# Performance work log

Measured on AMD Instinct MI355X. Metric: run time of the kernel, lower is better.

Reference implementation:

```python
import jax, jax.numpy as jnp
import numpy as np

KERNEL = 9
STRIDE = 2
NUM_ITERS = 3


def squash(s):
    # Matches the module: norm over last dim; v = ||s|| / (1 + ||s||^2) * s
    n = jnp.linalg.norm(s, axis=-1, keepdims=True)
    return n / (1.0 + n * n) * s


def setup_inputs() -> dict:
    key = jax.random.key(0)
    k1, k2, k3 = jax.random.split(key, 3)
    B, nc, ic, oc, H = 32, 32, 256, 32, 71  # H'=(71-9)//2+1 = 32 = B = nc = oc (required by the original broadcasting)
    x = jax.random.normal(k1, (B, ic, H, H), dtype=jnp.float32)
    # Conv2d default init: U(-1/sqrt(fan_in), 1/sqrt(fan_in)), fan_in = ic*9*9
    bound = 1.0 / np.sqrt(ic * KERNEL * KERNEL)
    W = jax.random.uniform(k2, (nc, oc, ic, KERNEL, KERNEL), jnp.float32, -bound, bound)
    b = jax.random.uniform(k3, (nc, oc), jnp.float32, -bound, bound)
    return {"x": x, "W": W, "b": b}


def reference(x, W, b):
    nc, oc, ic = W.shape[0], W.shape[1], W.shape[2]
    # All nc per-capsule convs fused into one grouped output-channel conv
    Wf = W.reshape(nc * oc, ic, KERNEL, KERNEL)
    u = jax.lax.conv_general_dilated(
        x, Wf, window_strides=(STRIDE, STRIDE), padding='VALID',
        dimension_numbers=('NCHW', 'OIHW', 'NCHW'))
    B = u.shape[0]
    Hp, Wp = u.shape[2], u.shape[3]
    u_hat = u.reshape(B, nc, oc, Hp, Wp) + b[None, :, :, None, None]  # [B,nc,oc,Hp,Wp]

    # Dynamic routing. The torch code initializes b_ij as rank-4 zeros; because
    # softmax(0) is uniform and 0 + agreement == agreement, this rank-5 zero init
    # is numerically identical and shape-clean.
    b_ij = jnp.zeros((B, nc, oc, Hp, 1), dtype=u_hat.dtype)
    v = None
    for it in range(NUM_ITERS):
        c = jax.nn.softmax(b_ij, axis=1)                  # over capsule dim
        s = (c * u_hat).sum(axis=2, keepdims=True)        # [B,nc,1,Hp,Wp]
        v = squash(s)
        if it < NUM_ITERS - 1:
            b_ij = b_ij + (u_hat * v).sum(axis=-1, keepdims=True)  # [B,nc,oc,Hp,1]
    # torch returns v_j.squeeze(-1): last dim is Wp != 1 so it is a no-op
    return v  # [B, nc, 1, Hp, Wp]
```

## Files before the change

### kernel.cpp

```cpp
#include <hip/hip_runtime.h>
#include <cstdint>
#include <cstddef>

typedef unsigned short u16;
typedef signed char s8;
typedef __attribute__((ext_vector_type(4))) int i32x4;

#define XT_HSTRIDE 18432
#define XT_BSTRIDE 1308672
#define K_TOT 20736
#define N_TOT 32768
#define NKT 324
#define S_X (5.0f / 127.0f)

__device__ __forceinline__ u16 f2bf(float f) {
  uint32_t u = __builtin_bit_cast(uint32_t, f);
  u = (u + 0x7fffu + ((u >> 16) & 1u)) >> 16;
  return (u16)u;
}
__device__ __forceinline__ float bf2f(u16 h) {
  uint32_t u = ((uint32_t)h) << 16;
  return __builtin_bit_cast(float, u);
}

__device__ __forceinline__ void gl_lds16(const s8* g, s8* l) {
  __builtin_amdgcn_global_load_lds((const __attribute__((address_space(1))) void*)g,
                                   (__attribute__((address_space(3))) void*)l, 16, 0, 0);
}

__device__ __forceinline__ void wg_barrier() {
  asm volatile("" ::: "memory");
  __builtin_amdgcn_s_barrier();
  asm volatile("" ::: "memory");
}

__device__ __forceinline__ void koffs(int kt, int& ka, int& kb) {
  const int pos = kt >> 2;
  const int cq = kt & 3;
  const int kh = pos / 9;
  const int kw = pos - kh * 9;
  ka = kt * 64;
  kb = kh * XT_HSTRIDE + (kw & 1) * 9216 + (kw >> 1) * 256 + cq * 64;
}

__global__ __launch_bounds__(256) void pack_w(const float* __restrict__ W,
                                              s8* __restrict__ Wb,
                                              float* __restrict__ sw) {
  __shared__ __align__(16) s8 wl[81 * 264];
  __shared__ float red[256];
  const int m = blockIdx.x;
  const int t = threadIdx.x;
  const size_t base = (size_t)m * K_TOT;
  float r[81];
  float mx = 0.f;
#pragma unroll
  for (int k = 0; k < 81; ++k) {
    r[k] = W[base + t + k * 256];
    mx = fmaxf(mx, fabsf(r[k]));
  }
  red[t] = mx;
  __syncthreads();
  for (int s = 128; s > 0; s >>= 1) {
    if (t < s) red[t] = fmaxf(red[t], red[t + s]);
    __syncthreads();
  }
  const float amax = fmaxf(red[0], 1e-20f);
  const float inv = 127.0f / amax;
  if (t == 0) sw[m] = amax * (1.0f / 127.0f);
#pragma unroll
  for (int k = 0; k < 81; ++k) {
    const int i = t + k * 256;
    const int c = i / 81;
    const int pos = i - c * 81;
    wl[pos * 264 + c] = (s8)__float2int_rn(r[k] * inv);
  }
  __syncthreads();
  for (int idx = t; idx < 81 * 32; idx += 256) {
    const int pos = idx >> 5;
    const int cq = idx & 31;
    *(uint2*)(Wb + base + pos * 256 + cq * 8) =
        *(const uint2*)(wl + pos * 264 + cq * 8);
  }
}

__global__ __launch_bounds__(256) void pack_x(const float* __restrict__ X,
                                              s8* __restrict__ xT) {
  __shared__ s8 xl[71 * 260];
  const int h = blockIdx.x;
  const int b = blockIdx.y;
  const int t = threadIdx.x;
  for (int i = t; i < 256 * 71; i += 256) {
    int c = i / 71;
    int w = i - c * 71;
    float f = X[(((size_t)(b * 256 + c)) * 71 + h) * 71 + w];
    f = fminf(fmaxf(f, -5.f), 5.f) * 25.4f;
    xl[w * 260 + c] = (s8)__float2int_rn(f);
  }
  __syncthreads();
  const size_t obase = (size_t)b * XT_BSTRIDE + (size_t)h * XT_HSTRIDE;
  const int c4 = t & 63;
  const int g = t >> 6;
  for (int s = g; s < 71; s += 4) {
    int par = (s >= 36) ? 1 : 0;
    int j = s - par * 36;
    int w = 2 * j + par;
    uint32_t d = *(const uint32_t*)&xl[w * 260 + 4 * c4];
    *(uint32_t*)&xT[obase + par * 9216 + j * 256 + 4 * c4] = d;
  }
}

__global__ __launch_bounds__(512, 2) void conv_gemm(const s8* __restrict__ Wb,
                                                    const s8* __restrict__ xT,
                                                    const float* __restrict__ sw,
                                                    u16* __restrict__ U) {
  __shared__ __align__(16) s8 As[2][2][256 * 64];
  __shared__ __align__(16) s8 Bs[2][2][256 * 64];
  const int tid = threadIdx.x;
  const int bx = blockIdx.x;
  const int swz = (bx & 7) * 64 + (bx >> 3);
  const int m0 = (swz & 3) * 256;
  const int n0 = (swz >> 2) * 256;
  const int lane = tid & 63;
  const int wave = tid >> 6;
  const int wm = wave >> 2;
  const int wn = wave & 3;

  const int rl2 = lane >> 2;
  const int gch16 = ((lane & 3) ^ ((rl2 >> 1) & 3)) * 16;

  const s8* aS[2];
  const s8* bS[2];
#pragma unroll
  for (int j = 0; j < 2; ++j) {
    const int row = j * 128 + wave * 16 + rl2;
    aS[j] = Wb + (size_t)(m0 + row) * K_TOT + gch16;
    const int n = n0 + row;
    const size_t nb = (size_t)(n >> 10) * XT_BSTRIDE +
                      (size_t)(((n >> 5) & 31) * 2) * XT_HSTRIDE +
                      (size_t)(n & 31) * 256;
    bS[j] = xT + nb + gch16;
  }
  const int sdst = wave * 16 * 64 + lane * 16;

  i32x4 acc[8][4];
#pragma unroll
  for (int i = 0; i < 8; ++i)
#pragma unroll
    for (int j = 0; j < 4; ++j) acc[i][j] = (i32x4){0, 0, 0, 0};

  const int fr = lane & 15;
  const int q4 = lane >> 4;
  const int cph = ((q4 ^ ((fr >> 1) & 3))) * 16;
  int offA[8], offB[4];
#pragma unroll
  for (int mi = 0; mi < 8; ++mi)
    offA[mi] = (wm * 128 + (mi & 3) * 16 + (mi >> 2) * 64 + fr) * 64 + cph;
#pragma unroll
  for (int j = 0; j < 4; ++j)
    offB[j] = (wn * 64 + j * 16 + fr) * 64 + cph;

  {
    int ka0, kb0, ka1, kb1;
    koffs(0, ka0, kb0);
    koffs(1, ka1, kb1);
    gl_lds16(bS[0] + kb0, &Bs[0][0][0 * 8192 + sdst]);
    gl_lds16(bS[1] + kb0, &Bs[0][0][1 * 8192 + sdst]);
    gl_lds16(bS[0] + kb1, &Bs[0][1][0 * 8192 + sdst]);
    gl_lds16(bS[1] + kb1, &Bs[0][1][1 * 8192 + sdst]);
    gl_lds16(aS[0] + ka0, &As[0][0][0 * 8192 + sdst]);
    gl_lds16(aS[1] + ka0, &As[0][0][1 * 8192 + sdst]);
    gl_lds16(aS[0] + ka1, &As[0][1][0 * 8192 + sdst]);
    gl_lds16(aS[1] + ka1, &As[0][1][1 * 8192 + sdst]);
  }

#pragma unroll 1
  for (int it2 = 0; it2 < NKT / 2; ++it2) {
    const int sp = it2 & 1;
    const bool more = (it2 + 1 < NKT / 2);
    int ka0n = 0, kb0n = 0, ka1n = 0, kb1n = 0;
    if (more) {
      koffs(2 * it2 + 2, ka0n, kb0n);
      koffs(2 * it2 + 3, ka1n, kb1n);
    }
    const s8* Ac0 = &As[sp][0][0];
    const s8* Bc0 = &Bs[sp][0][0];
    const s8* Ac1 = &As[sp][1][0];
    const s8* Bc1 = &Bs[sp][1][0];
    s8* An0 = &As[sp ^ 1][0][0];
    s8* Bn0 = &Bs[sp ^ 1][0][0];
    s8* An1 = &As[sp ^ 1][1][0];
    s8* Bn1 = &Bs[sp ^ 1][1][0];

    asm volatile("s_waitcnt vmcnt(0)" ::: "memory");
    wg_barrier();

    i32x4 aF[8], bF[4];

#pragma unroll
    for (int j = 0; j < 4; ++j) bF[j] = *(const i32x4*)(Bc0 + offB[j]);
#pragma unroll
    for (int mi = 0; mi < 4; ++mi) aF[mi] = *(const i32x4*)(Ac0 + offA[mi]);
    if (more) {
      gl_lds16(bS[0] + kb0n, Bn0 + 0 * 8192 + sdst);
      gl_lds16(bS[1] + kb0n, Bn0 + 1 * 8192 + sdst);
    }
    __builtin_amdgcn_s_setprio(1);
#pragma unroll
    for (int mi = 0; mi < 4; ++mi)
#pragma unroll
      for (int j = 0; j < 4; ++j)
        acc[mi][j] = __builtin_amdgcn_mfma_i32_16x16x64_i8(aF[mi], bF[j], acc[mi][j], 0, 0, 0);
    __builtin_amdgcn_s_setprio(0);
    __builtin_amdgcn_sched_barrier(0);

#pragma unroll
    for (int mi = 4; mi < 8; ++mi) aF[mi] = *(const i32x4*)(Ac0 + offA[mi]);
    if (more) {
      gl_lds16(bS[0] + kb1n, Bn1 + 0 * 8192 + sdst);
      gl_lds16(bS[1] + kb1n, Bn1 + 1 * 8192 + sdst);
    }
    __builtin_amdgcn_s_setprio(1);
#pragma unroll
    for (int mi = 4; mi < 8; ++mi)
#pragma unroll
      for (int j = 0; j < 4; ++j)
        acc[mi][j] = __builtin_amdgcn_mfma_i32_16x16x64_i8(aF[mi], bF[j], acc[mi][j], 0, 0, 0);
    __builtin_amdgcn_s_setprio(0);
    __builtin_amdgcn_sched_barrier(0);

#pragma unroll
    for (int j = 0; j < 4; ++j) bF[j] = *(const i32x4*)(Bc1 + offB[j]);
#pragma unroll
    for (int mi = 0; mi < 4; ++mi) aF[mi] = *(const i32x4*)(Ac1 + offA[mi]);
    if (more) {
      gl_lds16(aS[0] + ka0n, An0 + 0 * 8192 + sdst);
      gl_lds16(aS[1] + ka0n, An0 + 1 * 8192 + sdst);
    }
    __builtin_amdgcn_s_setprio(1);
#pragma unroll
    for (int mi = 0; mi < 4; ++mi)
#pragma unroll
      for (int j = 0; j < 4; ++j)
        acc[mi][j] = __builtin_amdgcn_mfma_i32_16x16x64_i8(aF[mi], bF[j], acc[mi][j], 0, 0, 0);
    __builtin_amdgcn_s_setprio(0);
    __builtin_amdgcn_sched_barrier(0);

#pragma unroll
    for (int mi = 4; mi < 8; ++mi) aF[mi] = *(const i32x4*)(Ac1 + offA[mi]);
    if (more) {
      gl_lds16(aS[0] + ka1n, An1 + 0 * 8192 + sdst);
      gl_lds16(aS[1] + ka1n, An1 + 1 * 8192 + sdst);
    }
    __builtin_amdgcn_s_setprio(1);
#pragma unroll
    for (int mi = 4; mi < 8; ++mi)
#pragma unroll
      for (int j = 0; j < 4; ++j)
        acc[mi][j] = __builtin_amdgcn_mfma_i32_16x16x64_i8(aF[mi], bF[j], acc[mi][j], 0, 0, 0);
    __builtin_amdgcn_s_setprio(0);
  }

  const int r0 = (lane >> 4) * 4;
  const int cn = lane & 15;
#pragma unroll
  for (int mi = 0; mi < 8; ++mi) {
    const int mgb = m0 + wm * 128 + (mi & 3) * 16 + (mi >> 2) * 64 + r0;
    float ds[4];
#pragma unroll
    for (int r = 0; r < 4; ++r) ds[r] = sw[mgb + r] * S_X;
#pragma unroll
    for (int j = 0; j < 4; ++j) {
      const int ng = n0 + wn * 64 + j * 16 + cn;
#pragma unroll
      for (int r = 0; r < 4; ++r)
        U[(size_t)(mgb + r) * N_TOT + ng] = f2bf((float)acc[mi][j][r] * ds[r]);
    }
  }
}

__global__ __launch_bounds__(1024) void routing_k(const u16* __restrict__ U,
                                                  const float* __restrict__ bias,
                                                  float* __restrict__ out) {
  const int t = threadIdx.x;
  const int bx = blockIdx.x;
  const int b = bx >> 5;
  const int hp = bx & 31;
  const int oc = t & 31;
  __shared__ float sm[1024];

  float u_r[32];
  {
    const uint4* up4 = (const uint4*)(U + (size_t)t * N_TOT + b * 1024 + hp * 32);
    const float bs = bias[t];
#pragma unroll
    for (int i = 0; i < 4; ++i) {
      uint4 q = up4[i];
      uint32_t vv[4] = {q.x, q.y, q.z, q.w};
#pragma unroll
      for (int k = 0; k < 4; ++k) {
        u_r[i * 8 + k * 2]     = bf2f((u16)(vv[k] & 0xffffu)) + bs;
        u_r[i * 8 + k * 2 + 1] = bf2f((u16)(vv[k] >> 16)) + bs;
      }
    }
  }

  float bij = 0.f;
  float s[32];
  float scale = 0.f;

  {
    const float c = 1.0f / 32.0f;
#pragma unroll
    for (int w = 0; w < 32; ++w) s[w] = c * u_r[w];
#pragma unroll
    for (int off = 1; off < 32; off <<= 1) {
#pragma unroll
      for (int w = 0; w < 32; ++w) s[w] += __shfl_xor(s[w], off, 64);
    }
    float n2 = 0.f;
#pragma unroll
    for (int w = 0; w < 32; ++w) n2 += s[w] * s[w];
    scale = sqrtf(n2) / (1.f + n2);
    float agr = 0.f;
#pragma unroll
    for (int w = 0; w < 32; ++w) agr += u_r[w] * s[w];
    bij += scale * agr;
  }

  for (int it = 1; it < 3; ++it) {
    sm[t] = __expf(bij);
    __syncthreads();
    float den = 0.f;
#pragma unroll
    for (int i = 0; i < 32; ++i) den += sm[i * 32 + oc];
    const float c = sm[t] / den;
#pragma unroll
    for (int w = 0; w < 32; ++w) s[w] = c * u_r[w];
#pragma unroll
    for (int off = 1; off < 32; off <<= 1) {
#pragma unroll
      for (int w = 0; w < 32; ++w) s[w] += __shfl_xor(s[w], off, 64);
    }
    float n2 = 0.f;
#pragma unroll
    for (int w = 0; w < 32; ++w) n2 += s[w] * s[w];
    scale = sqrtf(n2) / (1.f + n2);
    if (it < 2) {
      float agr = 0.f;
#pragma unroll
      for (int w = 0; w < 32; ++w) agr += u_r[w] * s[w];
      bij += scale * agr;
      __syncthreads();
    }
  }

  const int nc = t >> 5;
  float val = s[0];
#pragma unroll
  for (int i = 1; i < 32; ++i) val = (oc == i) ? s[i] : val;
  out[(size_t)((b * 32 + nc) * 32 + hp) * 32 + oc] = scale * val;
}

extern "C" void kernel_launch(void* const* d_in, const int* in_sizes, int n_in,
                              void* d_out, int out_size, void* d_ws, size_t ws_size,
                              hipStream_t stream) {
  const float* x = (const float*)d_in[0];
  const float* W = (const float*)d_in[1];
  const float* bias = (const float*)d_in[2];

  s8*    Wb = (s8*)d_ws;
  float* sw = (float*)((char*)d_ws + 21233664u);
  s8*    xT = (s8*)((char*)d_ws + 21237760u);
  u16*   U  = (u16*)((char*)d_ws + 63115264u);
  float* out = (float*)d_out;

  pack_w<<<dim3(1024), dim3(256), 0, stream>>>(W, Wb, sw);
  pack_x<<<dim3(71, 32), dim3(256), 0, stream>>>(x, xT);
  conv_gemm<<<dim3(512), dim3(512), 0, stream>>>(Wb, xT, sw, U);
  routing_k<<<dim3(1024), dim3(1024), 0, stream>>>(U, bias, out);
}
```

Before: 939.8 us.

## Switch conv GEMM to 32x32x32 int8 MFMA and merge pack kernels

The conv GEMM inner loop now issues 32x32x32 int8 MFMA instructions instead of 16x16x64. Each wave's 128x64 tile becomes 4x2 blocks of 16-register accumulators, and the LDS fragment offsets and epilogue row mapping are rewritten to match. The larger MFMA needs fewer fragment loads from LDS per multiply-add and fewer instructions issued. Separately, the weight and input pack kernels are merged into one launch to save a kernel launch and let the two run concurrently. The cost is a larger per-block shared memory footprint in the merged pack kernel, and the new epilogue writes shorter contiguous runs.

```diff
diff --git a/kernel.cpp b/kernel.cpp
--- a/kernel.cpp
+++ b/kernel.cpp
@@ -5,6 +5,7 @@
 typedef unsigned short u16;
 typedef signed char s8;
 typedef __attribute__((ext_vector_type(4))) int i32x4;
+typedef __attribute__((ext_vector_type(16))) int i32x16;
 
 #define XT_HSTRIDE 18432
 #define XT_BSTRIDE 1308672
@@ -43,69 +44,73 @@
   kb = kh * XT_HSTRIDE + (kw & 1) * 9216 + (kw >> 1) * 256 + cq * 64;
 }
 
-__global__ __launch_bounds__(256) void pack_w(const float* __restrict__ W,
-                                              s8* __restrict__ Wb,
-                                              float* __restrict__ sw) {
-  __shared__ __align__(16) s8 wl[81 * 264];
-  __shared__ float red[256];
-  const int m = blockIdx.x;
+__global__ __launch_bounds__(256) void pack_wx(const float* __restrict__ W,
+                                               const float* __restrict__ X,
+                                               s8* __restrict__ Wb,
+                                               float* __restrict__ sw,
+                                               s8* __restrict__ xT) {
+  __shared__ __align__(16) s8 smem[81 * 264 + 1024];
+  const int bx = blockIdx.x;
   const int t = threadIdx.x;
-  const size_t base = (size_t)m * K_TOT;
-  float r[81];
-  float mx = 0.f;
-#pragma unroll
-  for (int k = 0; k < 81; ++k) {
-    r[k] = W[base + t + k * 256];
-    mx = fmaxf(mx, fabsf(r[k]));
-  }
-  red[t] = mx;
-  __syncthreads();
-  for (int s = 128; s > 0; s >>= 1) {
-    if (t < s) red[t] = fmaxf(red[t], red[t + s]);
+
+  if (bx < 1024) {
+    s8* wl = smem;
+    float* red = (float*)(smem + 81 * 264);
+    const int m = bx;
+    const size_t base = (size_t)m * K_TOT;
+    float r[81];
+    float mx = 0.f;
+#pragma unroll
+    for (int k = 0; k < 81; ++k) {
+      r[k] = W[base + t + k * 256];
+      mx = fmaxf(mx, fabsf(r[k]));
+    }
+    red[t] = mx;
     __syncthreads();
-  }
-  const float amax = fmaxf(red[0], 1e-20f);
-  const float inv = 127.0f / amax;
-  if (t == 0) sw[m] = amax * (1.0f / 127.0f);
-#pragma unroll
-  for (int k = 0; k < 81; ++k) {
-    const int i = t + k * 256;
-    const int c = i / 81;
-    const int pos = i - c * 81;
-    wl[pos * 264 + c] = (s8)__float2int_rn(r[k] * inv);
-  }
-  __syncthreads();
-  for (int idx = t; idx < 81 * 32; idx += 256) {
-    const int pos = idx >> 5;
-    const int cq = idx & 31;
-    *(uint2*)(Wb + base + pos * 256 + cq * 8) =
-        *(const uint2*)(wl + pos * 264 + cq * 8);
-  }
-}
-
-__global__ __launch_bounds__(256) void pack_x(const float* __restrict__ X,
-                                              s8* __restrict__ xT) {
-  __shared__ s8 xl[71 * 260];
-  const int h = blockIdx.x;
-  const int b = blockIdx.y;
-  const int t = threadIdx.x;
-  for (int i = t; i < 256 * 71; i += 256) {
-    int c = i / 71;
-    int w = i - c * 71;
-    float f = X[(((size_t)(b * 256 + c)) * 71 + h) * 71 + w];
-    f = fminf(fmaxf(f, -5.f), 5.f) * 25.4f;
-    xl[w * 260 + c] = (s8)__float2int_rn(f);
-  }
-  __syncthreads();
-  const size_t obase = (size_t)b * XT_BSTRIDE + (size_t)h * XT_HSTRIDE;
-  const int c4 = t & 63;
-  const int g = t >> 6;
-  for (int s = g; s < 71; s += 4) {
-    int par = (s >= 36) ? 1 : 0;
-    int j = s - par * 36;
-    int w = 2 * j + par;
-    uint32_t d = *(const uint32_t*)&xl[w * 260 + 4 * c4];
-    *(uint32_t*)&xT[obase + par * 9216 + j * 256 + 4 * c4] = d;
+    for (int s = 128; s > 0; s >>= 1) {
+      if (t < s) red[t] = fmaxf(red[t], red[t + s]);
+      __syncthreads();
+    }
+    const float amax = fmaxf(red[0], 1e-20f);
+    const float inv = 127.0f / amax;
+    if (t == 0) sw[m] = amax * (1.0f / 127.0f);
+#pragma unroll
+    for (int k = 0; k < 81; ++k) {
+      const int i = t + k * 256;
+      const int c = i / 81;
+      const int pos = i - c * 81;
+      wl[pos * 264 + c] = (s8)__float2int_rn(r[k] * inv);
+    }
+    __syncthreads();
+    for (int idx = t; idx < 81 * 32; idx += 256) {
+      const int pos = idx >> 5;
+      const int cq = idx & 31;
+      *(uint2*)(Wb + base + pos * 256 + cq * 8) =
+          *(const uint2*)(wl + pos * 264 + cq * 8);
+    }
+  } else {
+    s8* xl = smem;
+    const int idx = bx - 1024;
+    const int h = idx % 71;
+    const int b = idx / 71;
+    for (int i = t; i < 256 * 71; i += 256) {
+      int c = i / 71;
+      int w = i - c * 71;
+      float f = X[(((size_t)(b * 256 + c)) * 71 + h) * 71 + w];
+      f = fminf(fmaxf(f, -5.f), 5.f) * 25.4f;
+      xl[w * 260 + c] = (s8)__float2int_rn(f);
+    }
+    __syncthreads();
+    const size_t obase = (size_t)b * XT_BSTRIDE + (size_t)h * XT_HSTRIDE;
+    const int c4 = t & 63;
+    const int g = t >> 6;
+    for (int s = g; s < 71; s += 4) {
+      int par = (s >= 36) ? 1 : 0;
+      int j = s - par * 36;
+      int w = 2 * j + par;
+      uint32_t d = *(const uint32_t*)&xl[w * 260 + 4 * c4];
+      *(uint32_t*)&xT[obase + par * 9216 + j * 256 + 4 * c4] = d;
+    }
   }
 }
 
@@ -142,22 +147,26 @@
   }
   const int sdst = wave * 16 * 64 + lane * 16;
 
-  i32x4 acc[8][4];
-#pragma unroll
-  for (int i = 0; i < 8; ++i)
-#pragma unroll
-    for (int j = 0; j < 4; ++j) acc[i][j] = (i32x4){0, 0, 0, 0};
-
-  const int fr = lane & 15;
-  const int q4 = lane >> 4;
-  const int cph = ((q4 ^ ((fr >> 1) & 3))) * 16;
-  int offA[8], offB[4];
-#pragma unroll
-  for (int mi = 0; mi < 8; ++mi)
-    offA[mi] = (wm * 128 + (mi & 3) * 16 + (mi >> 2) * 64 + fr) * 64 + cph;
-#pragma unroll
-  for (int j = 0; j < 4; ++j)
-    offB[j] = (wn * 64 + j * 16 + fr) * 64 + cph;
+  i32x16 acc[4][2];
+#pragma unroll
+  for (int i = 0; i < 4; ++i)
+#pragma unroll
+    for (int j = 0; j < 2; ++j) acc[i][j] = (i32x16)(0);
+
+  const int r31 = lane & 31;
+  const int kh5 = lane >> 5;
+  const int xr2 = (r31 >> 1) & 3;
+  int offA[4][2], offB[2][2];
+#pragma unroll
+  for (int mb = 0; mb < 4; ++mb)
+#pragma unroll
+    for (int ks = 0; ks < 2; ++ks)
+      offA[mb][ks] = (wm * 128 + mb * 32 + r31) * 64 + ((ks * 2 + kh5) ^ xr2) * 16;
+#pragma unroll
+  for (int nb = 0; nb < 2; ++nb)
+#pragma unroll
+    for (int ks = 0; ks < 2; ++ks)
+      offB[nb][ks] = (wn * 64 + nb * 32 + r31) * 64 + ((ks * 2 + kh5) ^ xr2) * 16;
 
   {
     int ka0, kb0, ka1, kb1;
@@ -194,86 +203,108 @@
     asm volatile("s_waitcnt vmcnt(0)" ::: "memory");
     wg_barrier();
 
-    i32x4 aF[8], bF[4];
-
-#pragma unroll
-    for (int j = 0; j < 4; ++j) bF[j] = *(const i32x4*)(Bc0 + offB[j]);
-#pragma unroll
-    for (int mi = 0; mi < 4; ++mi) aF[mi] = *(const i32x4*)(Ac0 + offA[mi]);
+    i32x4 aF[2][2], bF[2][2];
+
+#pragma unroll
+    for (int nb = 0; nb < 2; ++nb)
+#pragma unroll
+      for (int ks = 0; ks < 2; ++ks) bF[nb][ks] = *(const i32x4*)(Bc0 + offB[nb][ks]);
+#pragma unroll
+    for (int mb = 0; mb < 2; ++mb)
+#pragma unroll
+      for (int ks = 0; ks < 2; ++ks) aF[mb][ks] = *(const i32x4*)(Ac0 + offA[mb][ks]);
     if (more) {
       gl_lds16(bS[0] + kb0n, Bn0 + 0 * 8192 + sdst);
       gl_lds16(bS[1] + kb0n, Bn0 + 1 * 8192 + sdst);
     }
     __builtin_amdgcn_s_setprio(1);
 #pragma unroll
-    for (int mi = 0; mi < 4; ++mi)
-#pragma unroll
-      for (int j = 0; j < 4; ++j)
-        acc[mi][j] = __builtin_amdgcn_mfma_i32_16x16x64_i8(aF[mi], bF[j], acc[mi][j], 0, 0, 0);
+    for (int ks = 0; ks < 2; ++ks)
+#pragma unroll
+      for (int mb = 0; mb < 2; ++mb)
+#pragma unroll
+        for (int nb = 0; nb < 2; ++nb)
+          acc[mb][nb] = __builtin_amdgcn_mfma_i32_32x32x32_i8(aF[mb][ks], bF[nb][ks], acc[mb][nb], 0, 0, 0);
     __builtin_amdgcn_s_setprio(0);
     __builtin_amdgcn_sched_barrier(0);
 
 #pragma unroll
-    for (int mi = 4; mi < 8; ++mi) aF[mi] = *(const i32x4*)(Ac0 + offA[mi]);
+    for (int mb = 0; mb < 2; ++mb)
+#pragma unroll
+      for (int ks = 0; ks < 2; ++ks) aF[mb][ks] = *(const i32x4*)(Ac0 + offA[2 + mb][ks]);
     if (more) {
       gl_lds16(bS[0] + kb1n, Bn1 + 0 * 8192 + sdst);
       gl_lds16(bS[1] + kb1n, Bn1 + 1 * 8192 + sdst);
     }
     __builtin_amdgcn_s_setprio(1);
 #pragma unroll
-    for (int mi = 4; mi < 8; ++mi)
-#pragma unroll
-      for (int j = 0; j < 4; ++j)
-        acc[mi][j] = __builtin_amdgcn_mfma_i32_16x16x64_i8(aF[mi], bF[j], acc[mi][j], 0, 0, 0);
+    for (int ks = 0; ks < 2; ++ks)
+#pragma unroll
+      for (int mb = 0; mb < 2; ++mb)
+#pragma unroll
+        for (int nb = 0; nb < 2; ++nb)
+          acc[2 + mb][nb] = __builtin_amdgcn_mfma_i32_32x32x32_i8(aF[mb][ks], bF[nb][ks], acc[2 + mb][nb], 0, 0, 0);
     __builtin_amdgcn_s_setprio(0);
     __builtin_amdgcn_sched_barrier(0);
 
 #pragma unroll
-    for (int j = 0; j < 4; ++j) bF[j] = *(const i32x4*)(Bc1 + offB[j]);
-#pragma unroll
-    for (int mi = 0; mi < 4; ++mi) aF[mi] = *(const i32x4*)(Ac1 + offA[mi]);
+    for (int nb = 0; nb < 2; ++nb)
+#pragma unroll
+      for (int ks = 0; ks < 2; ++ks) bF[nb][ks] = *(const i32x4*)(Bc1 + offB[nb][ks]);
+#pragma unroll
+    for (int mb = 0; mb < 2; ++mb)
+#pragma unroll
+      for (int ks = 0; ks < 2; ++ks) aF[mb][ks] = *(const i32x4*)(Ac1 + offA[mb][ks]);
     if (more) {
       gl_lds16(aS[0] + ka0n, An0 + 0 * 8192 + sdst);
       gl_lds16(aS[1] + ka0n, An0 + 1 * 8192 + sdst);
     }
     __builtin_amdgcn_s_setprio(1);
 #pragma unroll
-    for (int mi = 0; mi < 4; ++mi)
-#pragma unroll
-      for (int j = 0; j < 4; ++j)
-        acc[mi][j] = __builtin_amdgcn_mfma_i32_16x16x64_i8(aF[mi], bF[j], acc[mi][j], 0, 0, 0);
+    for (int ks = 0; ks < 2; ++ks)
+#pragma unroll
+      for (int mb = 0; mb < 2; ++mb)
+#pragma unroll
+        for (int nb = 0; nb < 2; ++nb)
+          acc[mb][nb] = __builtin_amdgcn_mfma_i32_32x32x32_i8(aF[mb][ks], bF[nb][ks], acc[mb][nb], 0, 0, 0);
     __builtin_amdgcn_s_setprio(0);
     __builtin_amdgcn_sched_barrier(0);
 
 #pragma unroll
-    for (int mi = 4; mi < 8; ++mi) aF[mi] = *(const i32x4*)(Ac1 + offA[mi]);
+    for (int mb = 0; mb < 2; ++mb)
+#pragma unroll
+      for (int ks = 0; ks < 2; ++ks) aF[mb][ks] = *(const i32x4*)(Ac1 + offA[2 + mb][ks]);
     if (more) {
       gl_lds16(aS[0] + ka1n, An1 + 0 * 8192 + sdst);
       gl_lds16(aS[1] + ka1n, An1 + 1 * 8192 + sdst);
     }
     __builtin_amdgcn_s_setprio(1);
 #pragma unroll
-    for (int mi = 4; mi < 8; ++mi)
-#pragma unroll
-      for (int j = 0; j < 4; ++j)
-        acc[mi][j] = __builtin_amdgcn_mfma_i32_16x16x64_i8(aF[mi], bF[j], acc[mi][j], 0, 0, 0);
+    for (int ks = 0; ks < 2; ++ks)
+#pragma unroll
+      for (int mb = 0; mb < 2; ++mb)
+#pragma unroll
+        for (int nb = 0; nb < 2; ++nb)
+          acc[2 + mb][nb] = __builtin_amdgcn_mfma_i32_32x32x32_i8(aF[mb][ks], bF[nb][ks], acc[2 + mb][nb], 0, 0, 0);
     __builtin_amdgcn_s_setprio(0);
-  }
-
-  const int r0 = (lane >> 4) * 4;
-  const int cn = lane & 15;
-#pragma unroll
-  for (int mi = 0; mi < 8; ++mi) {
-    const int mgb = m0 + wm * 128 + (mi & 3) * 16 + (mi >> 2) * 64 + r0;
-    float ds[4];
-#pragma unroll
-    for (int r = 0; r < 4; ++r) ds[r] = sw[mgb + r] * S_X;
-#pragma unroll
-    for (int j = 0; j < 4; ++j) {
-      const int ng = n0 + wn * 64 + j * 16 + cn;
-#pragma unroll
-      for (int r = 0; r < 4; ++r)
-        U[(size_t)(mgb + r) * N_TOT + ng] = f2bf((float)acc[mi][j][r] * ds[r]);
+    __builtin_amdgcn_sched_barrier(0);
+  }
+
+  const int rh = 4 * kh5;
+#pragma unroll
+  for (int mb = 0; mb < 4; ++mb) {
+    const int mgb = m0 + wm * 128 + mb * 32 + rh;
+    float ds[16];
+#pragma unroll
+    for (int v = 0; v < 16; ++v) ds[v] = sw[mgb + (v & 3) + 8 * (v >> 2)] * S_X;
+#pragma unroll
+    for (int nb = 0; nb < 2; ++nb) {
+      const int ng = n0 + wn * 64 + nb * 32 + r31;
+#pragma unroll
+      for (int v = 0; v < 16; ++v) {
+        const int mg = mgb + (v & 3) + 8 * (v >> 2);
+        U[(size_t)mg * N_TOT + ng] = f2bf((float)acc[mb][nb][v] * ds[v]);
+      }
     }
   }
 }
@@ -374,8 +405,7 @@
   u16*   U  = (u16*)((char*)d_ws + 63115264u);
   float* out = (float*)d_out;
 
-  pack_w<<<dim3(1024), dim3(256), 0, stream>>>(W, Wb, sw);
-  pack_x<<<dim3(71, 32), dim3(256), 0, stream>>>(x, xT);
+  pack_wx<<<dim3(1024 + 71 * 32), dim3(256), 0, stream>>>(W, x, Wb, sw, xT);
   conv_gemm<<<dim3(512), dim3(512), 0, stream>>>(Wb, xT, sw, U);
   routing_k<<<dim3(1024), dim3(1024), 0, stream>>>(U, bias, out);
 }
```

Measured after the change: 1.004 ms. 1.07x slower.

## Merge weight/input pack kernels and split GEMM wait into half-step barriers

Applied to the files above, without the earlier changes.

Combines the two packing kernels into one launch whose blocks branch on block index, removing a launch and letting weight and input packing run concurrently. In the conv GEMM main loop, the prefetch order is changed so the next-stage k-slice-0 tiles (B then A) are issued first. The full vmcnt(0) wait is replaced with partial vmcnt(4) waits plus an extra mid-iteration barrier, so the second half-tile's loads can still be in flight while the first half is computed. This adds a barrier per iteration and depends on the vmcnt counts matching the issue order exactly.

```diff
diff --git a/kernel.cpp b/kernel.cpp
--- a/kernel.cpp
+++ b/kernel.cpp
@@ -43,69 +43,73 @@
   kb = kh * XT_HSTRIDE + (kw & 1) * 9216 + (kw >> 1) * 256 + cq * 64;
 }
 
-__global__ __launch_bounds__(256) void pack_w(const float* __restrict__ W,
-                                              s8* __restrict__ Wb,
-                                              float* __restrict__ sw) {
-  __shared__ __align__(16) s8 wl[81 * 264];
-  __shared__ float red[256];
-  const int m = blockIdx.x;
+__global__ __launch_bounds__(256) void pack_wx(const float* __restrict__ W,
+                                               const float* __restrict__ X,
+                                               s8* __restrict__ Wb,
+                                               float* __restrict__ sw,
+                                               s8* __restrict__ xT) {
+  __shared__ __align__(16) s8 smem[81 * 264 + 1024];
+  const int bx = blockIdx.x;
   const int t = threadIdx.x;
-  const size_t base = (size_t)m * K_TOT;
-  float r[81];
-  float mx = 0.f;
-#pragma unroll
-  for (int k = 0; k < 81; ++k) {
-    r[k] = W[base + t + k * 256];
-    mx = fmaxf(mx, fabsf(r[k]));
-  }
-  red[t] = mx;
-  __syncthreads();
-  for (int s = 128; s > 0; s >>= 1) {
-    if (t < s) red[t] = fmaxf(red[t], red[t + s]);
+
+  if (bx < 1024) {
+    s8* wl = smem;
+    float* red = (float*)(smem + 81 * 264);
+    const int m = bx;
+    const size_t base = (size_t)m * K_TOT;
+    float r[81];
+    float mx = 0.f;
+#pragma unroll
+    for (int k = 0; k < 81; ++k) {
+      r[k] = W[base + t + k * 256];
+      mx = fmaxf(mx, fabsf(r[k]));
+    }
+    red[t] = mx;
     __syncthreads();
-  }
-  const float amax = fmaxf(red[0], 1e-20f);
-  const float inv = 127.0f / amax;
-  if (t == 0) sw[m] = amax * (1.0f / 127.0f);
-#pragma unroll
-  for (int k = 0; k < 81; ++k) {
-    const int i = t + k * 256;
-    const int c = i / 81;
-    const int pos = i - c * 81;
-    wl[pos * 264 + c] = (s8)__float2int_rn(r[k] * inv);
-  }
-  __syncthreads();
-  for (int idx = t; idx < 81 * 32; idx += 256) {
-    const int pos = idx >> 5;
-    const int cq = idx & 31;
-    *(uint2*)(Wb + base + pos * 256 + cq * 8) =
-        *(const uint2*)(wl + pos * 264 + cq * 8);
-  }
-}
-
-__global__ __launch_bounds__(256) void pack_x(const float* __restrict__ X,
-                                              s8* __restrict__ xT) {
-  __shared__ s8 xl[71 * 260];
-  const int h = blockIdx.x;
-  const int b = blockIdx.y;
-  const int t = threadIdx.x;
-  for (int i = t; i < 256 * 71; i += 256) {
-    int c = i / 71;
-    int w = i - c * 71;
-    float f = X[(((size_t)(b * 256 + c)) * 71 + h) * 71 + w];
-    f = fminf(fmaxf(f, -5.f), 5.f) * 25.4f;
-    xl[w * 260 + c] = (s8)__float2int_rn(f);
-  }
-  __syncthreads();
-  const size_t obase = (size_t)b * XT_BSTRIDE + (size_t)h * XT_HSTRIDE;
-  const int c4 = t & 63;
-  const int g = t >> 6;
-  for (int s = g; s < 71; s += 4) {
-    int par = (s >= 36) ? 1 : 0;
-    int j = s - par * 36;
-    int w = 2 * j + par;
-    uint32_t d = *(const uint32_t*)&xl[w * 260 + 4 * c4];
-    *(uint32_t*)&xT[obase + par * 9216 + j * 256 + 4 * c4] = d;
+    for (int s = 128; s > 0; s >>= 1) {
+      if (t < s) red[t] = fmaxf(red[t], red[t + s]);
+      __syncthreads();
+    }
+    const float amax = fmaxf(red[0], 1e-20f);
+    const float inv = 127.0f / amax;
+    if (t == 0) sw[m] = amax * (1.0f / 127.0f);
+#pragma unroll
+    for (int k = 0; k < 81; ++k) {
+      const int i = t + k * 256;
+      const int c = i / 81;
+      const int pos = i - c * 81;
+      wl[pos * 264 + c] = (s8)__float2int_rn(r[k] * inv);
+    }
+    __syncthreads();
+    for (int idx = t; idx < 81 * 32; idx += 256) {
+      const int pos = idx >> 5;
+      const int cq = idx & 31;
+      *(uint2*)(Wb + base + pos * 256 + cq * 8) =
+          *(const uint2*)(wl + pos * 264 + cq * 8);
+    }
+  } else {
+    s8* xl = smem;
+    const int idx = bx - 1024;
+    const int h = idx % 71;
+    const int b = idx / 71;
+    for (int i = t; i < 256 * 71; i += 256) {
+      int c = i / 71;
+      int w = i - c * 71;
+      float f = X[(((size_t)(b * 256 + c)) * 71 + h) * 71 + w];
+      f = fminf(fmaxf(f, -5.f), 5.f) * 25.4f;
+      xl[w * 260 + c] = (s8)__float2int_rn(f);
+    }
+    __syncthreads();
+    const size_t obase = (size_t)b * XT_BSTRIDE + (size_t)h * XT_HSTRIDE;
+    const int c4 = t & 63;
+    const int g = t >> 6;
+    for (int s = g; s < 71; s += 4) {
+      int par = (s >= 36) ? 1 : 0;
+      int j = s - par * 36;
+      int w = 2 * j + par;
+      uint32_t d = *(const uint32_t*)&xl[w * 260 + 4 * c4];
+      *(uint32_t*)&xT[obase + par * 9216 + j * 256 + 4 * c4] = d;
+    }
   }
 }
 
@@ -165,10 +169,10 @@
     koffs(1, ka1, kb1);
     gl_lds16(bS[0] + kb0, &Bs[0][0][0 * 8192 + sdst]);
     gl_lds16(bS[1] + kb0, &Bs[0][0][1 * 8192 + sdst]);
+    gl_lds16(aS[0] + ka0, &As[0][0][0 * 8192 + sdst]);
+    gl_lds16(aS[1] + ka0, &As[0][0][1 * 8192 + sdst]);
     gl_lds16(bS[0] + kb1, &Bs[0][1][0 * 8192 + sdst]);
     gl_lds16(bS[1] + kb1, &Bs[0][1][1 * 8192 + sdst]);
-    gl_lds16(aS[0] + ka0, &As[0][0][0 * 8192 + sdst]);
-    gl_lds16(aS[1] + ka0, &As[0][0][1 * 8192 + sdst]);
     gl_lds16(aS[0] + ka1, &As[0][1][0 * 8192 + sdst]);
     gl_lds16(aS[1] + ka1, &As[0][1][1 * 8192 + sdst]);
   }
@@ -191,7 +195,7 @@
     s8* An1 = &As[sp ^ 1][1][0];
     s8* Bn1 = &Bs[sp ^ 1][1][0];
 
-    asm volatile("s_waitcnt vmcnt(0)" ::: "memory");
+    asm volatile("s_waitcnt vmcnt(4)" ::: "memory");
     wg_barrier();
 
     i32x4 aF[8], bF[4];
@@ -216,8 +220,8 @@
 #pragma unroll
     for (int mi = 4; mi < 8; ++mi) aF[mi] = *(const i32x4*)(Ac0 + offA[mi]);
     if (more) {
-      gl_lds16(bS[0] + kb1n, Bn1 + 0 * 8192 + sdst);
-      gl_lds16(bS[1] + kb1n, Bn1 + 1 * 8192 + sdst);
+      gl_lds16(aS[0] + ka0n, An0 + 0 * 8192 + sdst);
+      gl_lds16(aS[1] + ka0n, An0 + 1 * 8192 + sdst);
     }
     __builtin_amdgcn_s_setprio(1);
 #pragma unroll
@@ -228,13 +232,20 @@
     __builtin_amdgcn_s_setprio(0);
     __builtin_amdgcn_sched_barrier(0);
 
+    if (more) {
+      asm volatile("s_waitcnt vmcnt(4)" ::: "memory");
+    } else {
+      asm volatile("s_waitcnt vmcnt(0)" ::: "memory");
+    }
+    wg_barrier();
+
 #pragma unroll
     for (int j = 0; j < 4; ++j) bF[j] = *(const i32x4*)(Bc1 + offB[j]);
 #pragma unroll
     for (int mi = 0; mi < 4; ++mi) aF[mi] = *(const i32x4*)(Ac1 + offA[mi]);
     if (more) {
-      gl_lds16(aS[0] + ka0n, An0 + 0 * 8192 + sdst);
-      gl_lds16(aS[1] + ka0n, An0 + 1 * 8192 + sdst);
+      gl_lds16(bS[0] + kb1n, Bn1 + 0 * 8192 + sdst);
+      gl_lds16(bS[1] + kb1n, Bn1 + 1 * 8192 + sdst);
     }
     __builtin_amdgcn_s_setprio(1);
 #pragma unroll
@@ -258,6 +269,7 @@
       for (int j = 0; j < 4; ++j)
         acc[mi][j] = __builtin_amdgcn_mfma_i32_16x16x64_i8(aF[mi], bF[j], acc[mi][j], 0, 0, 0);
     __builtin_amdgcn_s_setprio(0);
+    __builtin_amdgcn_sched_barrier(0);
   }
 
   const int r0 = (lane >> 4) * 4;
@@ -374,8 +386,7 @@
   u16*   U  = (u16*)((char*)d_ws + 63115264u);
   float* out = (float*)d_out;
 
-  pack_w<<<dim3(1024), dim3(256), 0, stream>>>(W, Wb, sw);
-  pack_x<<<dim3(71, 32), dim3(256), 0, stream>>>(x, xT);
+  pack_wx<<<dim3(1024 + 71 * 32), dim3(256), 0, stream>>>(W, x, Wb, sw, xT);
   conv_gemm<<<dim3(512), dim3(512), 0, stream>>>(Wb, xT, sw, U);
   routing_k<<<dim3(1024), dim3(1024), 0, stream>>>(U, bias, out);
 }
```

New measurement: 953.7 us. About the same (+1.5%).
